# Kernel tuning notes

Hardware: AMD Instinct MI355X
Metric: run time of the kernel (lower is better)

The kernel has to match this reference:

```python
import jax, jax.numpy as jnp
import numpy as np

NUM_HEADS = 16
CAUSAL = True


def setup_inputs() -> dict:
    key = jax.random.key(0)
    ks = jax.random.split(key, 3)
    B, T, D = 2, 2048, 1024
    s = 1.0 / np.sqrt(D)
    return {
        "x": jax.random.normal(ks[0], (B, T, D), dtype=jnp.float32),
        "W_qkv": jax.random.normal(ks[1], (3 * D, D), dtype=jnp.float32) * s,
        "b_qkv": jnp.zeros((3 * D,), dtype=jnp.float32),
        "W_out": jax.random.normal(ks[2], (D, D), dtype=jnp.float32) * s,
        "b_out": jnp.zeros((D,), dtype=jnp.float32),
    }


def reference(x, W_qkv, b_qkv, W_out, b_out):
    B, T, D = x.shape
    H = NUM_HEADS
    hd = D // H
    # qkv projection: torch Linear y = x @ W.T + b
    qkv = jnp.einsum('btd,ed->bte', x, W_qkv) + b_qkv  # [B,T,3D]
    qkv = qkv.reshape(B, T, H, 3 * hd).transpose(0, 2, 1, 3)  # [B,H,T,3hd]
    q, k, v = jnp.split(qkv, 3, axis=-1)  # each [B,H,T,hd]
    scale = 1.0 / np.sqrt(hd).astype(np.float32)
    scores = jnp.einsum('bhtd,bhsd->bhts', q, k) * scale  # [B,H,T,T]
    if CAUSAL:
        mask = jnp.triu(jnp.ones((T, T), dtype=bool), k=1)
        scores = jnp.where(mask, jnp.float32(-jnp.inf), scores)
    weights = jax.nn.softmax(scores, axis=-1)
    attn = jnp.einsum('bhts,bhsd->bhtd', weights, v)  # [B,H,T,hd]
    out = attn.transpose(0, 2, 1, 3).reshape(B, T, D)
    return jnp.einsum('btd,ed->bte', out, W_out) + b_out
```

## Files before the change

kernel.cpp:

```cpp
#include <hip/hip_runtime.h>
#include <hip/hip_bf16.h>
#include <cstdint>


using short8  = __attribute__((ext_vector_type(8))) short;
using floatx4 = __attribute__((ext_vector_type(4))) float;

#define LDS_STRIDE 40

__device__ __forceinline__ float bf16_to_f32(unsigned short u) {
    union { unsigned int i; float f; } v; v.i = ((unsigned int)u) << 16; return v.f;
}
__device__ __forceinline__ unsigned short f32_to_bf16(float f) {
    union { float f; unsigned int i; } v; v.f = f;
    unsigned int x = v.i;
    unsigned int r = x + 0x7FFFu + ((x >> 16) & 1u);
    return (unsigned short)(r >> 16);
}
__device__ __forceinline__ unsigned short f32_to_bf16_fast(float f) {
    union { float f; unsigned int i; } v; v.f = f;
    return (unsigned short)((v.i + 0x8000u) >> 16);
}
__device__ __forceinline__ short8 cvt8(const float* __restrict__ p) {
    const float4 f0 = *(const float4*)p;
    const float4 f1 = *(const float4*)(p + 4);
    short8 r;
    r[0] = (short)f32_to_bf16(f0.x); r[1] = (short)f32_to_bf16(f0.y);
    r[2] = (short)f32_to_bf16(f0.z); r[3] = (short)f32_to_bf16(f0.w);
    r[4] = (short)f32_to_bf16(f1.x); r[5] = (short)f32_to_bf16(f1.y);
    r[6] = (short)f32_to_bf16(f1.z); r[7] = (short)f32_to_bf16(f1.w);
    return r;
}
__device__ __forceinline__ unsigned int cvtpk(float a, float b) {
    unsigned int r;
    asm("v_cvt_pk_bf16_f32 %0, %1, %2" : "=v"(r) : "v"(a), "v"(b));
    return r;
}

#define Q_PRESCALE 0.1803368801111204f

#if __has_builtin(__builtin_amdgcn_global_load_lds)
#define ASYNC_STAGE 1
typedef const __attribute__((address_space(1))) void* gas1_t;
typedef __attribute__((address_space(3))) void* las3_t;
#else
#define ASYNC_STAGE 0
#endif

__device__ __forceinline__ void gload_lds16(const ushort* g, ushort* l) {
#if ASYNC_STAGE
    __builtin_amdgcn_global_load_lds((gas1_t)g, (las3_t)l, 16, 0, 0);
#else
    *(short8*)l = *(const short8*)g;
#endif
}

__global__ __launch_bounds__(256, 8) void cvt_bf16(
    const float* __restrict__ in, ushort* __restrict__ out, int n8)
{
    const int i = blockIdx.x * 256 + threadIdx.x;
    if (i < n8) *(short8*)(out + (size_t)i * 8) = cvt8(in + (size_t)i * 8);
}

template <int MODE>
__global__ __launch_bounds__(256, 3) void gemm_bf16(
    const ushort* __restrict__ A, const ushort* __restrict__ W,
    const float* __restrict__ bias,
    ushort* __restrict__ Cq, ushort* __restrict__ Ck, ushort* __restrict__ Cv,
    float* __restrict__ Cout, int M, int N, int K)
{
    __shared__ __align__(16) ushort As[128 * 32];
    __shared__ __align__(16) ushort Bs[128 * 32];

    const int tid  = threadIdx.x;
    const int lane = tid & 63;
    const int wave = tid >> 6;
    const int wm = (wave >> 1) * 64;
    const int wn = (wave & 1) * 64;
    const int m0 = blockIdx.x * 128;
    const int n0 = blockIdx.y * 128;
    const int quad = lane >> 4;
    const int l16  = lane & 15;

    floatx4 acc[4][4];
#pragma unroll
    for (int i = 0; i < 4; i++)
#pragma unroll
        for (int j = 0; j < 4; j++) acc[i][j] = (floatx4)0.0f;

    const int srow = wave * 16 + (lane >> 2);
    const int scol = (lane & 3) * 8;
    ushort* ldsA0 = &As[wave * 512];
    ushort* ldsA1 = &As[2048 + wave * 512];
    ushort* ldsB0 = &Bs[wave * 512];
    ushort* ldsB1 = &Bs[2048 + wave * 512];
    const ushort* pA0 = A + (size_t)(m0 + srow) * K + scol;
    const ushort* pA1 = pA0 + (size_t)64 * K;
    const ushort* pB0 = W + (size_t)(n0 + srow) * K + scol;
    const ushort* pB1 = pB0 + (size_t)64 * K;

    for (int k0 = 0; k0 < K; k0 += 32) {
#if ASYNC_STAGE
        __syncthreads();
        gload_lds16(pA0 + k0, ldsA0);
        gload_lds16(pA1 + k0, ldsA1);
        gload_lds16(pB0 + k0, ldsB0);
        gload_lds16(pB1 + k0, ldsB1);
        __syncthreads();
#else
        const short8 a0 = *(const short8*)(pA0 + k0);
        const short8 a1 = *(const short8*)(pA1 + k0);
        const short8 b0 = *(const short8*)(pB0 + k0);
        const short8 b1 = *(const short8*)(pB1 + k0);
        __syncthreads();
        *(short8*)&As[srow * 32 + scol] = a0;
        *(short8*)&As[(srow + 64) * 32 + scol] = a1;
        *(short8*)&Bs[srow * 32 + scol] = b0;
        *(short8*)&Bs[(srow + 64) * 32 + scol] = b1;
        __syncthreads();
#endif

        short8 af[4], bf[4];
#pragma unroll
        for (int i = 0; i < 4; i++)
            af[i] = *(const short8*)&As[(wm + i * 16 + l16) * 32 + quad * 8];
#pragma unroll
        for (int j = 0; j < 4; j++)
            bf[j] = *(const short8*)&Bs[(wn + j * 16 + l16) * 32 + quad * 8];
#pragma unroll
        for (int i = 0; i < 4; i++)
#pragma unroll
            for (int j = 0; j < 4; j++)
                acc[i][j] = __builtin_amdgcn_mfma_f32_16x16x32_bf16(af[i], bf[j], acc[i][j], 0, 0, 0);
    }

#pragma unroll
    for (int i = 0; i < 4; i++) {
#pragma unroll
        for (int j = 0; j < 4; j++) {
#pragma unroll
            for (int r = 0; r < 4; r++) {
                const int row = m0 + wm + i * 16 + quad * 4 + r;
                const int col = n0 + wn + j * 16 + l16;
                float v = acc[i][j][r] + bias[col];
                if (MODE == 0) {
                    const int h  = col / 192;
                    const int rr = col - h * 192;
                    const int sel = rr >> 6;
                    const int d   = rr & 63;
                    const int b = row >> 11;
                    const int t = row & 2047;
                    const size_t idx = (((size_t)(b * 16 + h)) * 2048 + t) * 64 + d;
                    if (sel == 0)      Cq[idx] = f32_to_bf16(v * Q_PRESCALE);
                    else if (sel == 1) Ck[idx] = f32_to_bf16(v);
                    else               Cv[idx] = f32_to_bf16(v);
                } else {
                    Cout[(size_t)row * N + col] = v;
                }
            }
        }
    }
}

template <int MODE, int AFP32>
__global__ __launch_bounds__(256, 2) void gemm_bt(
    const void* __restrict__ Av, const float* __restrict__ W,
    const float* __restrict__ bias,
    ushort* __restrict__ Cq, ushort* __restrict__ Ck, ushort* __restrict__ Cv,
    float* __restrict__ Cout, int M, int N, int K)
{
    __shared__ __align__(16) ushort As[128 * LDS_STRIDE];
    __shared__ __align__(16) ushort Bs[128 * LDS_STRIDE];

    const int tid  = threadIdx.x;
    const int lane = tid & 63;
    const int wave = tid >> 6;
    const int wm = (wave >> 1) * 64;
    const int wn = (wave & 1) * 64;
    const int m0 = blockIdx.x * 128;
    const int n0 = blockIdx.y * 128;
    const int quad = lane >> 4;
    const int l16  = lane & 15;

    floatx4 acc[4][4];
#pragma unroll
    for (int i = 0; i < 4; i++)
#pragma unroll
        for (int j = 0; j < 4; j++) acc[i][j] = (floatx4)0.0f;

    const int srow = tid >> 2;
    const int scol = (tid & 3) * 8;

    for (int k0 = 0; k0 < K; k0 += 32) {
        short8 a0, a1;
        if (AFP32) {
            const float* A = (const float*)Av;
            a0 = cvt8(A + (size_t)(m0 + srow) * K + k0 + scol);
            a1 = cvt8(A + (size_t)(m0 + srow + 64) * K + k0 + scol);
        } else {
            const ushort* A = (const ushort*)Av;
            a0 = *(const short8*)(A + (size_t)(m0 + srow) * K + k0 + scol);
            a1 = *(const short8*)(A + (size_t)(m0 + srow + 64) * K + k0 + scol);
        }
        const short8 b0 = cvt8(W + (size_t)(n0 + srow) * K + k0 + scol);
        const short8 b1 = cvt8(W + (size_t)(n0 + srow + 64) * K + k0 + scol);
        __syncthreads();
        *(short8*)&As[srow * LDS_STRIDE + scol] = a0;
        *(short8*)&As[(srow + 64) * LDS_STRIDE + scol] = a1;
        *(short8*)&Bs[srow * LDS_STRIDE + scol] = b0;
        *(short8*)&Bs[(srow + 64) * LDS_STRIDE + scol] = b1;
        __syncthreads();

        short8 af[4], bf[4];
#pragma unroll
        for (int i = 0; i < 4; i++)
            af[i] = *(const short8*)&As[(wm + i * 16 + l16) * LDS_STRIDE + quad * 8];
#pragma unroll
        for (int j = 0; j < 4; j++)
            bf[j] = *(const short8*)&Bs[(wn + j * 16 + l16) * LDS_STRIDE + quad * 8];
#pragma unroll
        for (int i = 0; i < 4; i++)
#pragma unroll
            for (int j = 0; j < 4; j++)
                acc[i][j] = __builtin_amdgcn_mfma_f32_16x16x32_bf16(af[i], bf[j], acc[i][j], 0, 0, 0);
    }

#pragma unroll
    for (int i = 0; i < 4; i++) {
#pragma unroll
        for (int j = 0; j < 4; j++) {
#pragma unroll
            for (int r = 0; r < 4; r++) {
                const int row = m0 + wm + i * 16 + quad * 4 + r;
                const int col = n0 + wn + j * 16 + l16;
                float v = acc[i][j][r] + bias[col];
                if (MODE == 0) {
                    const int h  = col / 192;
                    const int rr = col - h * 192;
                    const int sel = rr >> 6;
                    const int d   = rr & 63;
                    const int b = row >> 11;
                    const int t = row & 2047;
                    const size_t idx = (((size_t)(b * 16 + h)) * 2048 + t) * 64 + d;
                    if (sel == 0)      Cq[idx] = f32_to_bf16(v * Q_PRESCALE);
                    else if (sel == 1) Ck[idx] = f32_to_bf16(v);
                    else               Cv[idx] = f32_to_bf16(v);
                } else {
                    Cout[(size_t)row * N + col] = v;
                }
            }
        }
    }
}

__global__ __launch_bounds__(256, 4) void transpose_v(
    const ushort* __restrict__ V, ushort* __restrict__ Vt)
{
    const int bh = blockIdx.x & 31;
    const int tt = blockIdx.x >> 5;
    const int t0 = tt * 64;
    const int tid = threadIdx.x;
    __shared__ __align__(16) ushort tile[64 * 72];

    const int r = tid >> 2, c = (tid & 3) * 16;
    const ushort* src = V + ((size_t)bh * 2048 + t0 + r) * 64 + c;
    *(short8*)&tile[r * 72 + c]     = *(const short8*)src;
    *(short8*)&tile[r * 72 + c + 8] = *(const short8*)(src + 8);
    __syncthreads();

    const int w = tid >> 6, lane = tid & 63;
    const int d  = w * 16 + (lane >> 2);
    const int tc = (lane & 3) * 16;
    __attribute__((aligned(16))) ushort out[16];
#pragma unroll
    for (int i = 0; i < 16; i++) {
        const int slot = (tc & 31) + i;
        const int key  = ((slot >> 2) & 1) * 16 + ((slot >> 3) & 3) * 4 + (slot & 3);
        out[i] = tile[((tc & 32) + key) * 72 + d];
    }
    ushort* dst = Vt + ((size_t)(bh * 32 + tt) * 64 + d) * 64 + tc;
    *(short8*)dst       = *(const short8*)&out[0];
    *(short8*)(dst + 8) = *(const short8*)&out[8];
}

__global__ __launch_bounds__(256, 2) void attn_mfma(
    const ushort* __restrict__ Q, const ushort* __restrict__ K,
    const ushort* __restrict__ Vtb, ushort* __restrict__ O)
{
    const int bid   = blockIdx.x;
    const int bh    = bid & 31;
    const int qtIdx = bid >> 5;
    const int qt    = (qtIdx < 8) ? (15 - qtIdx) : (qtIdx - 8);
    const int tid  = threadIdx.x;
    const int wave = tid >> 6;
    const int lane = tid & 63;
    const int quad = lane >> 4;
    const int l16  = lane & 15;
    const int qb   = qt * 128 + wave * 32;

    __shared__ __align__(16) ushort Ks[4096];
    __shared__ __align__(16) ushort Vs[4096];

    const size_t kbase = (size_t)bh * 2048 * 64;

    const int ob0 = tid * 16, ob1 = ob0 + 4096;
    const int r0 = ob0 >> 7, c0 = (ob0 >> 4) & 7;
    const int r1 = ob1 >> 7, c1 = (ob1 >> 4) & 7;
    const int e0 = r0 * 64 + ((c0 ^ (r0 & 7)) << 3);
    const int e1 = r1 * 64 + ((c1 ^ (r1 & 7)) << 3);
    ushort* dK0 = &Ks[wave * 512];
    ushort* dK1 = &Ks[2048 + wave * 512];
    ushort* dV0 = &Vs[wave * 512];
    ushort* dV1 = &Vs[2048 + wave * 512];
    const ushort* Kb = K + kbase;
    const ushort* Vb = Vtb + (size_t)bh * 32 * 4096;

    const int sw0 = ((quad ^ (l16 & 7)) << 3);
    const int sw1 = (((4 + quad) ^ (l16 & 7)) << 3);
    const int rbase = l16 * 64;

    short8 qf0[2], qf1[2];
#pragma unroll
    for (int f = 0; f < 2; f++) {
        const ushort* qp = Q + kbase + (size_t)(qb + f * 16 + l16) * 64 + quad * 8;
        qf0[f] = *(const short8*)qp;
        qf1[f] = *(const short8*)(qp + 32);
    }

    floatx4 accO[2][4];
#pragma unroll
    for (int f = 0; f < 2; f++)
#pragma unroll
        for (int d = 0; d < 4; d++) accO[f][d] = (floatx4)0.0f;
    float accLs[2] = {0.0f, 0.0f};

    union PB { unsigned int u[4]; short8 s8; };

    const int nt = 2 * qt + 2;
    for (int t = 0; t < nt; ++t) {
        __syncthreads();
        const ushort* Ktile = Kb + t * 4096;
        const ushort* Vtile = Vb + t * 4096;
        gload_lds16(Ktile + e0, dK0);
        gload_lds16(Ktile + e1, dK1);
        gload_lds16(Vtile + e0, dV0);
        gload_lds16(Vtile + e1, dV1);
        __syncthreads();

        short8 kf[4][2], vf[4][2];
#pragma unroll
        for (int j = 0; j < 4; j++) {
            kf[j][0] = *(const short8*)&Ks[j * 1024 + rbase + sw0];
            kf[j][1] = *(const short8*)&Ks[j * 1024 + rbase + sw1];
        }
#pragma unroll
        for (int d = 0; d < 4; d++) {
            vf[d][0] = *(const short8*)&Vs[d * 1024 + rbase + sw0];
            vf[d][1] = *(const short8*)&Vs[d * 1024 + rbase + sw1];
        }

#pragma unroll
        for (int f = 0; f < 2; f++) {
            const int qlo = qb + f * 16;
            if (t * 64 > qlo + 15) continue;
            floatx4 s[4];
#pragma unroll
            for (int j = 0; j < 4; j++) {
                floatx4 acc = (floatx4)0.0f;
                acc = __builtin_amdgcn_mfma_f32_16x16x32_bf16(kf[j][0], qf0[f], acc, 0, 0, 0);
                acc = __builtin_amdgcn_mfma_f32_16x16x32_bf16(kf[j][1], qf1[f], acc, 0, 0, 0);
                s[j] = acc;
            }
            if (t * 64 + 63 > qlo) {
                const int qcol = qlo + l16;
#pragma unroll
                for (int j = 0; j < 4; j++) {
                    const int keyb = t * 64 + j * 16 + quad * 4;
#pragma unroll
                    for (int r = 0; r < 4; r++)
                        if (keyb + r > qcol) s[j][r] = -1e30f;
                }
            }
#pragma unroll
            for (int j = 0; j < 4; j++)
#pragma unroll
                for (int r = 0; r < 4; r++)
                    s[j][r] = __builtin_amdgcn_exp2f(s[j][r]);
            const floatx4 ssum = s[0] + s[1] + s[2] + s[3];
            accLs[f] += (ssum[0] + ssum[1]) + (ssum[2] + ssum[3]);
            PB p0, p1;
#pragma unroll
            for (int j = 0; j < 2; j++) {
                p0.u[j * 2 + 0] = cvtpk(s[j][0], s[j][1]);
                p0.u[j * 2 + 1] = cvtpk(s[j][2], s[j][3]);
                p1.u[j * 2 + 0] = cvtpk(s[j + 2][0], s[j + 2][1]);
                p1.u[j * 2 + 1] = cvtpk(s[j + 2][2], s[j + 2][3]);
            }
#pragma unroll
            for (int d = 0; d < 4; d++) {
                accO[f][d] = __builtin_amdgcn_mfma_f32_16x16x32_bf16(p0.s8, vf[d][0], accO[f][d], 0, 0, 0);
                accO[f][d] = __builtin_amdgcn_mfma_f32_16x16x32_bf16(p1.s8, vf[d][1], accO[f][d], 0, 0, 0);
            }
        }
    }

    const int b = bh >> 4, h = bh & 15;
#pragma unroll
    for (int f = 0; f < 2; f++) {
        float L = accLs[f];
        L += __shfl_xor(L, 16);
        L += __shfl_xor(L, 32);
        float inv[4];
#pragma unroll
        for (int r = 0; r < 4; r++) inv[r] = 1.0f / __shfl(L, quad * 4 + r);
#pragma unroll
        for (int d = 0; d < 4; d++)
#pragma unroll
            for (int r = 0; r < 4; r++)
                O[(size_t)(b * 2048 + qb + f * 16 + quad * 4 + r) * 1024 + h * 64 + d * 16 + l16] =
                    f32_to_bf16(accO[f][d][r] * inv[r]);
    }
}

extern "C" void kernel_launch(void* const* d_in, const int* in_sizes, int n_in,
                              void* d_out, int out_size, void* d_ws, size_t ws_size,
                              hipStream_t stream) {
    const float* x    = (const float*)d_in[0];
    const float* Wqkv = (const float*)d_in[1];
    const float* bqkv = (const float*)d_in[2];
    const float* Wout = (const float*)d_in[3];
    const float* bout = (const float*)d_in[4];
    float* out = (float*)d_out;

    char* ws = (char*)d_ws;
    const size_t MB = 1024 * 1024;
    ushort* Q    = (ushort*)(ws + 0 * MB);
    ushort* Kk   = (ushort*)(ws + 8 * MB);
    ushort* Vt   = (ushort*)(ws + 16 * MB);
    ushort* rawV = (ushort*)(ws + 24 * MB);
    ushort* O    = (ushort*)(ws + 24 * MB);

    const dim3 blk(256);
    if (ws_size >= 48 * MB) {
        ushort* xb    = (ushort*)(ws + 32 * MB);
        ushort* Wqkvb = (ushort*)(ws + 40 * MB);
        ushort* Woutb = (ushort*)(ws + 46 * MB);
        cvt_bf16<<<dim3(2048), blk, 0, stream>>>(x, xb, 524288);
        cvt_bf16<<<dim3(1536), blk, 0, stream>>>(Wqkv, Wqkvb, 393216);
        cvt_bf16<<<dim3(512),  blk, 0, stream>>>(Wout, Woutb, 131072);
        gemm_bf16<0><<<dim3(32, 24), blk, 0, stream>>>(xb, Wqkvb, bqkv, Q, Kk, rawV,
                                                       nullptr, 4096, 3072, 1024);
        transpose_v<<<dim3(1024), blk, 0, stream>>>(rawV, Vt);
        attn_mfma<<<dim3(512), blk, 0, stream>>>(Q, Kk, Vt, O);
        gemm_bf16<1><<<dim3(32, 8), blk, 0, stream>>>(O, Woutb, bout, nullptr, nullptr,
                                                      nullptr, out, 4096, 1024, 1024);
    } else {
        gemm_bt<0, 1><<<dim3(32, 24), blk, 0, stream>>>(x, Wqkv, bqkv, Q, Kk, rawV,
                                                        nullptr, 4096, 3072, 1024);
        transpose_v<<<dim3(1024), blk, 0, stream>>>(rawV, Vt);
        attn_mfma<<<dim3(512), blk, 0, stream>>>(Q, Kk, Vt, O);
        gemm_bt<1, 0><<<dim3(32, 8), blk, 0, stream>>>(O, Wout, bout, nullptr, nullptr,
                                                       nullptr, out, 4096, 1024, 1024);
    }
}
```

Before: 184.3 us.

## Double-buffer K/V tiles in attention and merge three bf16 conversion launches

The attention kernel now keeps two LDS buffers for K and V and issues the async global-to-LDS load of the next tile before computing on the current one, with one barrier per iteration instead of two. This aims to hide global load latency behind MFMA work. Separately, the three fp32-to-bf16 conversion kernels are fused into one launch that branches on index range, removing two kernel launches. Doubling the LDS per block may reduce occupancy.

```diff
diff --git a/kernel.cpp b/kernel.cpp
--- a/kernel.cpp
+++ b/kernel.cpp
@@ -55,11 +55,17 @@
 #endif
 }
 
-__global__ __launch_bounds__(256, 8) void cvt_bf16(
-    const float* __restrict__ in, ushort* __restrict__ out, int n8)
+__global__ __launch_bounds__(256, 8) void cvt_bf16_3(
+    const float* __restrict__ x,  const float* __restrict__ wq,
+    const float* __restrict__ wo, ushort* __restrict__ xb,
+    ushort* __restrict__ wqb, ushort* __restrict__ wob)
 {
     const int i = blockIdx.x * 256 + threadIdx.x;
-    if (i < n8) *(short8*)(out + (size_t)i * 8) = cvt8(in + (size_t)i * 8);
+    const float* src; ushort* dst; int off;
+    if (i < 524288)      { src = x;  dst = xb;  off = i; }
+    else if (i < 917504) { src = wq; dst = wqb; off = i - 524288; }
+    else                 { src = wo; dst = wob; off = i - 917504; }
+    *(short8*)(dst + (size_t)off * 8) = cvt8(src + (size_t)off * 8);
 }
 
 template <int MODE>
@@ -298,8 +304,8 @@
     const int l16  = lane & 15;
     const int qb   = qt * 128 + wave * 32;
 
-    __shared__ __align__(16) ushort Ks[4096];
-    __shared__ __align__(16) ushort Vs[4096];
+    __shared__ __align__(16) ushort Ks[2][4096];
+    __shared__ __align__(16) ushort Vs[2][4096];
 
     const size_t kbase = (size_t)bh * 2048 * 64;
 
@@ -308,12 +314,17 @@
     const int r1 = ob1 >> 7, c1 = (ob1 >> 4) & 7;
     const int e0 = r0 * 64 + ((c0 ^ (r0 & 7)) << 3);
     const int e1 = r1 * 64 + ((c1 ^ (r1 & 7)) << 3);
-    ushort* dK0 = &Ks[wave * 512];
-    ushort* dK1 = &Ks[2048 + wave * 512];
-    ushort* dV0 = &Vs[wave * 512];
-    ushort* dV1 = &Vs[2048 + wave * 512];
     const ushort* Kb = K + kbase;
     const ushort* Vb = Vtb + (size_t)bh * 32 * 4096;
+
+    auto stage = [&](int t, ushort* KsB, ushort* VsB) {
+        const ushort* Ktile = Kb + t * 4096;
+        const ushort* Vtile = Vb + t * 4096;
+        gload_lds16(Ktile + e0, KsB + wave * 512);
+        gload_lds16(Ktile + e1, KsB + 2048 + wave * 512);
+        gload_lds16(Vtile + e0, VsB + wave * 512);
+        gload_lds16(Vtile + e1, VsB + 2048 + wave * 512);
+    };
 
     const int sw0 = ((quad ^ (l16 & 7)) << 3);
     const int sw1 = (((4 + quad) ^ (l16 & 7)) << 3);
@@ -336,27 +347,17 @@
 
     union PB { unsigned int u[4]; short8 s8; };
 
-    const int nt = 2 * qt + 2;
-    for (int t = 0; t < nt; ++t) {
-        __syncthreads();
-        const ushort* Ktile = Kb + t * 4096;
-        const ushort* Vtile = Vb + t * 4096;
-        gload_lds16(Ktile + e0, dK0);
-        gload_lds16(Ktile + e1, dK1);
-        gload_lds16(Vtile + e0, dV0);
-        gload_lds16(Vtile + e1, dV1);
-        __syncthreads();
-
+    auto compute = [&](int t, const ushort* KsB, const ushort* VsB) {
         short8 kf[4][2], vf[4][2];
 #pragma unroll
         for (int j = 0; j < 4; j++) {
-            kf[j][0] = *(const short8*)&Ks[j * 1024 + rbase + sw0];
-            kf[j][1] = *(const short8*)&Ks[j * 1024 + rbase + sw1];
+            kf[j][0] = *(const short8*)&KsB[j * 1024 + rbase + sw0];
+            kf[j][1] = *(const short8*)&KsB[j * 1024 + rbase + sw1];
         }
 #pragma unroll
         for (int d = 0; d < 4; d++) {
-            vf[d][0] = *(const short8*)&Vs[d * 1024 + rbase + sw0];
-            vf[d][1] = *(const short8*)&Vs[d * 1024 + rbase + sw1];
+            vf[d][0] = *(const short8*)&VsB[d * 1024 + rbase + sw0];
+            vf[d][1] = *(const short8*)&VsB[d * 1024 + rbase + sw1];
         }
 
 #pragma unroll
@@ -402,6 +403,21 @@
                 accO[f][d] = __builtin_amdgcn_mfma_f32_16x16x32_bf16(p1.s8, vf[d][1], accO[f][d], 0, 0, 0);
             }
         }
+    };
+
+    const int nt = 2 * qt + 2;
+    stage(0, Ks[0], Vs[0]);
+    __syncthreads();
+    int t = 0;
+    while (true) {
+        if (t + 1 < nt) stage(t + 1, Ks[1], Vs[1]);
+        compute(t, Ks[0], Vs[0]);
+        __syncthreads();
+        if (++t >= nt) break;
+        if (t + 1 < nt) stage(t + 1, Ks[0], Vs[0]);
+        compute(t, Ks[1], Vs[1]);
+        __syncthreads();
+        if (++t >= nt) break;
     }
 
     const int b = bh >> 4, h = bh & 15;
@@ -445,9 +461,7 @@
         ushort* xb    = (ushort*)(ws + 32 * MB);
         ushort* Wqkvb = (ushort*)(ws + 40 * MB);
         ushort* Woutb = (ushort*)(ws + 46 * MB);
-        cvt_bf16<<<dim3(2048), blk, 0, stream>>>(x, xb, 524288);
-        cvt_bf16<<<dim3(1536), blk, 0, stream>>>(Wqkv, Wqkvb, 393216);
-        cvt_bf16<<<dim3(512),  blk, 0, stream>>>(Wout, Woutb, 131072);
+        cvt_bf16_3<<<dim3(4096), blk, 0, stream>>>(x, Wqkv, Wout, xb, Wqkvb, Woutb);
         gemm_bf16<0><<<dim3(32, 24), blk, 0, stream>>>(xb, Wqkvb, bqkv, Q, Kk, rawV,
                                                        nullptr, 4096, 3072, 1024);
         transpose_v<<<dim3(1024), blk, 0, stream>>>(rawV, Vt);
```

Result: faster. 177.5 us (-3.7%).
